# Performance work log

Measured on AMD Instinct MI355X. Metric: run time of the kernel, lower is better.

## Reference

```python
import jax, jax.numpy as jnp
import numpy as np

V, L, D, DEMO, HID, N = 20000, 128, 256, 70, 1024, 2048


def setup_inputs() -> dict:
    key = jax.random.key(0)
    ks = jax.random.split(key, 16)
    s = 1.0 / np.sqrt(D)
    inp = {
        # learned parameters
        "E": jax.random.normal(ks[0], (V, D), jnp.float32) * 0.02,
        "Wq": jax.random.normal(ks[1], (D, D), jnp.float32) * s,
        "Wk": jax.random.normal(ks[2], (D, D), jnp.float32) * s,
        "Wv": jax.random.normal(ks[3], (D, D), jnp.float32) * s,
        "c_attn": jnp.ones((1,), jnp.float32) * 0.1,   # time_weight_net coefficient (attention decay)
        "c_pool": jnp.ones((1,), jnp.float32) * 0.5,   # history_repr Q_base-style pooling decay
        "W1": jax.random.normal(ks[4], (D + DEMO, HID), jnp.float32) * (1.0 / np.sqrt(D + DEMO)),
        "b1": jnp.zeros((HID,), jnp.float32),
        "W2": jax.random.normal(ks[5], (HID, 1), jnp.float32) * (1.0 / np.sqrt(HID)),
        "b2": jnp.zeros((1,), jnp.float32),
        # batched ragged task instances
        "demo": jax.random.normal(ks[6], (N, DEMO), jnp.float32),
        "hist_times": jax.random.uniform(ks[7], (N, L), jnp.float32) * 10.0,
        "event_time": jax.random.uniform(ks[8], (N,), jnp.float32) * 10.0 + 10.0,
        "labels": jax.random.randint(ks[9], (N,), 0, 2).astype(jnp.float32),
        "codes": jax.random.randint(ks[10], (N, L), 0, V),
        "lengths": jax.random.randint(ks[11], (N,), 1, L + 1).astype(jnp.int32),
    }
    return inp


def reference(E, Wq, Wk, Wv, c_attn, c_pool, W1, b1, W2, b2,
              demo, hist_times, event_time, labels, codes, lengths):
    POS_WEIGHT = 2.0
    NEG = jnp.float32(-1e9)
    mask = jnp.arange(L)[None, :] < lengths[:, None]            # [N, L] valid history positions

    emb = E[codes]                                              # [N, L, D] gather
    q = jnp.einsum('nld,de->nle', emb, Wq)
    k = jnp.einsum('nld,de->nle', emb, Wk)
    v = jnp.einsum('nld,de->nle', emb, Wv)

    # time-aware self-attention over each ragged history (masked)
    scores = jnp.einsum('nid,njd->nij', q, k) / jnp.sqrt(jnp.float32(D))
    dt = jnp.abs(hist_times[:, :, None] - hist_times[:, None, :])  # [N, L, L]
    scores = scores - c_attn[0] * dt
    scores = jnp.where(mask[:, None, :], scores, NEG)
    attn = jax.nn.softmax(scores, axis=-1)
    events = jnp.einsum('nij,njd->nid', attn, v)                # [N, L, D]

    # history_repr: time-decayed pooling toward event_time
    w = -c_pool[0] * (event_time[:, None] - hist_times)         # [N, L]
    w = jnp.where(mask, w, NEG)
    w = jax.nn.softmax(w, axis=-1)
    repr_ = jnp.einsum('nl,nld->nd', w, events)                 # [N, D]

    # disease/death classifier: demographics + history repr -> logit
    x = jnp.concatenate([demo, repr_], axis=-1)                 # [N, DEMO+D]
    h = jax.nn.relu(x @ W1 + b1)
    logit = (h @ W2 + b2)[:, 0]                                 # [N]

    # BCEWithLogitsLoss with pos_weight, averaged over valid predictions
    loss = -(POS_WEIGHT * labels * jax.nn.log_sigmoid(logit)
             + (1.0 - labels) * jax.nn.log_sigmoid(-logit))
    avg_loss = jnp.mean(loss)

    reg_loss = jnp.sum(c_attn ** 2) + jnp.sum(c_pool ** 2)      # time_weight_net.get_reg_loss()
    return avg_loss + reg_loss
```

## Files before the change

kernel.cpp:

```cpp
#include <hip/hip_runtime.h>
#include <hip/hip_bf16.h>
#include <math.h>
#include <stdint.h>

#define VV 20000
#define LL 128
#define DD 256
#define DEMO_ 70
#define HID_ 1024
#define NN 2048

typedef __attribute__((ext_vector_type(8))) short short8;
typedef __attribute__((ext_vector_type(4))) float f32x4;

__device__ __forceinline__ float bf2f(uint32_t u) {
    union { uint32_t u; float f; } c; c.u = u << 16; return c.f;
}
__device__ __forceinline__ uint32_t f2bf(float f) {
    union { float f; uint32_t u; } c; c.f = f;
    return (c.u + 0x7fffu + ((c.u >> 16) & 1u)) >> 16;
}

__device__ __forceinline__ int sw_off(int row, int col) {
    return (row << 8) + ((((col >> 3) ^ (row & 7)) << 3) | (col & 7));
}

__global__ __launch_bounds__(256) void k_pre(
    const float* __restrict__ Wq, const float* __restrict__ Wk,
    const float* __restrict__ Wv, const float* __restrict__ W1,
    const float* __restrict__ ca, const float* __restrict__ cp,
    const int* __restrict__ lens,
    unsigned short* __restrict__ Mxf, unsigned short* __restrict__ W1f,
    int* __restrict__ order, float* __restrict__ z,
    int* __restrict__ tickets, float* __restrict__ out)
{
    __shared__ float sm[DD];
    __shared__ float wvs[8][DD];
    __shared__ int cnt[9], off[9], cur[9];
    const int b = blockIdx.x, t = threadIdx.x;

    if (b < 256) {
        int e = b;
        sm[t] = Wq[(size_t)e * DD + t];
        __syncthreads();
        const float4* wk4 = (const float4*)(Wk + (size_t)t * DD);
        const float4* wq4 = (const float4*)sm;
        float4 acc = make_float4(0.f, 0.f, 0.f, 0.f);
        #pragma unroll 8
        for (int c = 0; c < DD / 4; ++c) {
            float4 a = wq4[c]; float4 bb = wk4[c];
            acc.x += a.x * bb.x; acc.y += a.y * bb.y;
            acc.z += a.z * bb.z; acc.w += a.w * bb.w;
        }
        float val = acc.x + acc.y + acc.z + acc.w;
        int frag = (e >> 4) * 8 + (t >> 5);
        int pos  = (((t >> 3) & 3) * 16 + (e & 15)) * 8 + (t & 7);
        Mxf[(size_t)frag * 512 + pos] = (unsigned short)f2bf(val);
    } else if (b < 384) {
        int f = b - 256, kg = f >> 2, hh = f & 3;
        #pragma unroll
        for (int r = 0; r < 8; ++r)
            wvs[r][t] = Wv[(size_t)(kg * 8 + r) * DD + t];
        __syncthreads();
        int h = hh * 256 + t;
        float acc[8];
        #pragma unroll
        for (int r = 0; r < 8; ++r) acc[r] = 0.f;
        #pragma unroll 4
        for (int n = 0; n < DD; ++n) {
            float a = W1[(size_t)(DEMO_ + n) * HID_ + h];
            #pragma unroll
            for (int r = 0; r < 8; ++r) acc[r] += wvs[r][n] * a;
        }
        #pragma unroll
        for (int r = 0; r < 8; ++r) {
            int k = DEMO_ + kg * 8 + r;
            int frag = (h >> 4) * 11 + (k >> 5);
            int pos  = (((k >> 3) & 3) * 16 + (h & 15)) * 8 + (k & 7);
            W1f[(size_t)frag * 512 + pos] = (unsigned short)f2bf(acc[r]);
        }
    } else if (b < 416) {
        int g = b - 384;
        for (int idx = g * 256 + t; idx < 96 * 1024; idx += 32 * 256) {
            int kk = idx >> 10, h = idx & 1023;
            int k = kk < DEMO_ ? kk : kk + 256;
            float val = kk < DEMO_ ? W1[(size_t)kk * HID_ + h] : 0.f;
            int frag = (h >> 4) * 11 + (k >> 5);
            int pos  = (((k >> 3) & 3) * 16 + (h & 15)) * 8 + (k & 7);
            W1f[(size_t)frag * 512 + pos] = (unsigned short)f2bf(val);
        }
    } else {
        for (int i = t; i < NN; i += 256) z[i] = 0.f;
        if (t < 128) tickets[t] = 0;
        if (t < 9) cnt[t] = 0;
        __syncthreads();
        for (int i = t; i < NN; i += 256)
            atomicAdd(&cnt[(lens[i] + 15) >> 4], 1);
        __syncthreads();
        if (t == 0) {
            int acc = 0;
            for (int k = 8; k >= 1; --k) { off[k] = acc; acc += cnt[k]; cur[k] = off[k]; }
            out[0] = ca[0] * ca[0] + cp[0] * cp[0];
        }
        __syncthreads();
        for (int i = t; i < NN; i += 256) {
            int key = (lens[i] + 15) >> 4;
            int pos = atomicAdd(&cur[key], 1);
            order[pos] = i;
        }
    }
}

__global__ __launch_bounds__(512, 4) void k_main(
    const float* __restrict__ E,
    const float* __restrict__ ht,  const float* __restrict__ evt_t,
    const int* __restrict__ codes, const int* __restrict__ lens,
    const float* __restrict__ ca_p, const float* __restrict__ cp_p,
    const unsigned short* __restrict__ Mxf,
    const int* __restrict__ order,
    unsigned short* __restrict__ Rbf)
{
    __shared__ __align__(16) unsigned short emb_u[LL * DD];
    __shared__ float times_s[LL];
    __shared__ int   codes_s[LL];
    __shared__ float w_s[LL];
    __shared__ float apart[8][LL];
    __shared__ float rp_part[8][DD];
    __shared__ float asum[LL];

    const int n = order[blockIdx.x];
    const int tid = threadIdx.x, wv = tid >> 6, ln = tid & 63;
    const int q = ln >> 4, m = ln & 15;
    const int len = lens[n];
    const int it_n = (len + 15) >> 4;
    const float ca = ca_p[0], cp = cp_p[0];
    const float evt = evt_t[n];

    short8 bB[2][8];
    #pragma unroll
    for (int nt = 0; nt < 2; ++nt)
        #pragma unroll
        for (int kk = 0; kk < 8; ++kk)
            bB[nt][kk] = *(const short8*)(Mxf + (size_t)((wv * 2 + nt) * 8 + kk) * 512 + ln * 8);

    if (tid < LL) {
        bool v = tid < len;
        times_s[tid] = v ? ht[(size_t)n * LL + tid] : 0.f;
        codes_s[tid] = v ? codes[(size_t)n * LL + tid] : 0;
    }
    if (wv == 0) {
        float t0 = (ln      < len) ? ht[(size_t)n * LL + ln]      : 0.f;
        float t1 = (ln + 64 < len) ? ht[(size_t)n * LL + ln + 64] : 0.f;
        float e0 = (ln      < len) ? __expf(cp * (t0 - evt)) : 0.f;
        float e1 = (ln + 64 < len) ? __expf(cp * (t1 - evt)) : 0.f;
        float smm = e0 + e1;
        for (int o = 32; o; o >>= 1) smm += __shfl_xor(smm, o, 64);
        float inv = 1.f / smm;
        if (ln      < len) w_s[ln]      = e0 * inv;
        if (ln + 64 < len) w_s[ln + 64] = e1 * inv;
    }
    __syncthreads();

    for (int l0 = wv; l0 < len; l0 += 32) {
        float4 v[4];
        #pragma unroll
        for (int u = 0; u < 4; ++u) {
            int l = l0 + u * 8;
            if (l < len)
                v[u] = ((const float4*)(E + (size_t)codes_s[l] * DD))[ln];
        }
        #pragma unroll
        for (int u = 0; u < 4; ++u) {
            int l = l0 + u * 8;
            if (l < len)
                *(uint2*)&emb_u[sw_off(l, 4 * ln)] =
                    make_uint2(f2bf(v[u].x) | (f2bf(v[u].y) << 16),
                               f2bf(v[u].z) | (f2bf(v[u].w) << 16));
        }
    }
    __syncthreads();

    short8 aC[8];
    for (int it = 0; it < it_n; ++it) {
        f32x4 h0 = (f32x4)0.f, h1 = (f32x4)0.f;
        #pragma unroll
        for (int kk = 0; kk < 8; ++kk) {
            short8 af = *(const short8*)&emb_u[sw_off(it * 16 + m, kk * 32 + q * 8)];
            if (it == wv) aC[kk] = af;
            h0 = __builtin_amdgcn_mfma_f32_16x16x32_bf16(af, bB[0][kk], h0, 0, 0, 0);
            h1 = __builtin_amdgcn_mfma_f32_16x16x32_bf16(af, bB[1][kk], h1, 0, 0, 0);
        }
        __syncthreads();
        #pragma unroll
        for (int r = 0; r < 4; ++r) {
            int row = it * 16 + q * 4 + r;
            emb_u[sw_off(row, wv * 32 + m)]      = (unsigned short)f2bf(h0[r]);
            emb_u[sw_off(row, wv * 32 + 16 + m)] = (unsigned short)f2bf(h1[r]);
        }
    }
    __syncthreads();

    if (wv < it_n) {
        f32x4 sac[8];
        #pragma unroll
        for (int jt = 0; jt < 8; ++jt) sac[jt] = (f32x4)0.f;
        for (int jt = 0; jt < it_n; ++jt) {
            #pragma unroll
            for (int kk = 0; kk < 8; ++kk) {
                short8 bH = *(const short8*)&emb_u[sw_off(jt * 16 + m, kk * 32 + q * 8)];
                sac[jt] = __builtin_amdgcn_mfma_f32_16x16x32_bf16(aC[kk], bH, sac[jt], 0, 0, 0);
            }
        }
        int i_base = wv * 16 + q * 4;
        float ti[4]; bool vR[4]; float rowsum[4];
        #pragma unroll
        for (int r = 0; r < 4; ++r) {
            vR[r] = (i_base + r) < len;
            ti[r] = times_s[i_base + r];
            rowsum[r] = 0.f;
        }
        for (int jt = 0; jt < it_n; ++jt) {
            int jcol = jt * 16 + m;
            bool vC = jcol < len;
            float tj = times_s[jcol];
            #pragma unroll
            for (int r = 0; r < 4; ++r) {
                float arg = sac[jt][r] * 0.0625f - ca * fabsf(ti[r] - tj);
                float p = (vR[r] && vC) ? __expf(arg) : 0.f;
                sac[jt][r] = p;
                rowsum[r] += p;
            }
        }
        #pragma unroll
        for (int r = 0; r < 4; ++r) {
            float s = rowsum[r];
            s += __shfl_xor(s, 1, 64); s += __shfl_xor(s, 2, 64);
            s += __shfl_xor(s, 4, 64); s += __shfl_xor(s, 8, 64);
            rowsum[r] = s;
        }
        float sc[4];
        #pragma unroll
        for (int r = 0; r < 4; ++r)
            sc[r] = (vR[r] && rowsum[r] > 0.f) ? w_s[i_base + r] / rowsum[r] : 0.f;
        for (int jt = 0; jt < it_n; ++jt) {
            float v = sc[0] * sac[jt][0] + sc[1] * sac[jt][1]
                    + sc[2] * sac[jt][2] + sc[3] * sac[jt][3];
            v += __shfl_xor(v, 16, 64);
            v += __shfl_xor(v, 32, 64);
            if (q == 0) apart[wv][jt * 16 + m] = v;
        }
    }
    __syncthreads();

    if (tid < LL) {
        float s = 0.f;
        for (int r = 0; r < it_n; ++r) s += apart[r][tid];
        asum[tid] = s;
    }
    __syncthreads();

    if (wv < it_n) {
        float aw = asum[wv * 16 + m];
        #pragma unroll
        for (int kk = 0; kk < 8; ++kk) {
            float v[8];
            #pragma unroll
            for (int j = 0; j < 8; ++j)
                v[j] = aw * bf2f((uint32_t)(unsigned short)aC[kk][j]);
            #pragma unroll
            for (int o = 1; o <= 8; o <<= 1)
                #pragma unroll
                for (int j = 0; j < 8; ++j)
                    v[j] += __shfl_xor(v[j], o, 64);
            if (m < 8)
                rp_part[wv][kk * 32 + q * 8 + m] = v[m];
        }
    }
    __syncthreads();
    if (tid < DD) {
        float r = 0.f;
        for (int t2 = 0; t2 < it_n; ++t2) r += rp_part[t2][tid];
        Rbf[(size_t)n * DD + tid] = (unsigned short)f2bf(r);
    }
}

__global__ __launch_bounds__(256) void k_mlp(
    const float* __restrict__ demo, const float* __restrict__ labels,
    const float* __restrict__ b1,   const float* __restrict__ W2,
    const float* __restrict__ b2,
    const unsigned short* __restrict__ Rbf,
    const unsigned short* __restrict__ W1f,
    float* __restrict__ z, int* __restrict__ tickets,
    float* __restrict__ out)
{
    __shared__ __align__(16) unsigned short xs[16][360];
    __shared__ float W2s[256];
    __shared__ float b1s[256];
    __shared__ float wred[4][16];
    __shared__ int   lastflag;

    const int tid = threadIdx.x, wv = tid >> 6, ln = tid & 63;
    const int q = ln >> 4, m = ln & 15;
    const int sg = blockIdx.x;
    const int s0 = sg * 16;
    const int by = blockIdx.y;
    const int hbase = by * 256;

    W2s[tid] = W2[hbase + tid];
    b1s[tid] = b1[hbase + tid];
    {
        int sh = tid >> 6, lane = tid & 63;
        for (int s = sh; s < 16; s += 4) {
            int n_s = s0 + s;
            const uint32_t* rsrc = (const uint32_t*)(Rbf + (size_t)n_s * DD);
            ((uint32_t*)&xs[s][DEMO_])[lane]      = rsrc[lane];
            ((uint32_t*)&xs[s][DEMO_])[lane + 64] = rsrc[lane + 64];
            if (lane < 35) {
                float2 d = ((const float2*)(demo + (size_t)n_s * DEMO_))[lane];
                xs[s][2 * lane]     = (unsigned short)f2bf(d.x);
                xs[s][2 * lane + 1] = (unsigned short)f2bf(d.y);
            }
            if (lane < 17) ((uint32_t*)&xs[s][326])[lane] = 0;
        }
    }
    __syncthreads();

    f32x4 cacc[4];
    #pragma unroll
    for (int ntl = 0; ntl < 4; ++ntl) cacc[ntl] = (f32x4)0.f;

    for (int kk = 0; kk < 11; ++kk) {
        short8 af = *(const short8*)&xs[m][kk * 32 + q * 8];
        #pragma unroll
        for (int ntl = 0; ntl < 4; ++ntl) {
            int frag = (by * 16 + wv * 4 + ntl) * 11 + kk;
            short8 bfd = *(const short8*)(W1f + (size_t)frag * 512 + ln * 8);
            cacc[ntl] = __builtin_amdgcn_mfma_f32_16x16x32_bf16(af, bfd, cacc[ntl], 0, 0, 0);
        }
    }

    float ls0 = 0.f, ls1 = 0.f, ls2 = 0.f, ls3 = 0.f;
    #pragma unroll
    for (int ntl = 0; ntl < 4; ++ntl) {
        int hl = wv * 64 + ntl * 16 + m;
        float bb = b1s[hl], w2v = W2s[hl];
        ls0 += fmaxf(cacc[ntl][0] + bb, 0.f) * w2v;
        ls1 += fmaxf(cacc[ntl][1] + bb, 0.f) * w2v;
        ls2 += fmaxf(cacc[ntl][2] + bb, 0.f) * w2v;
        ls3 += fmaxf(cacc[ntl][3] + bb, 0.f) * w2v;
    }
    #pragma unroll
    for (int o = 1; o <= 8; o <<= 1) {
        ls0 += __shfl_xor(ls0, o, 64); ls1 += __shfl_xor(ls1, o, 64);
        ls2 += __shfl_xor(ls2, o, 64); ls3 += __shfl_xor(ls3, o, 64);
    }
    if (m == 0) {
        wred[wv][q * 4 + 0] = ls0; wred[wv][q * 4 + 1] = ls1;
        wred[wv][q * 4 + 2] = ls2; wred[wv][q * 4 + 3] = ls3;
    }
    __syncthreads();
    if (tid < 16)
        atomicAdd(&z[s0 + tid], wred[0][tid] + wred[1][tid] + wred[2][tid] + wred[3][tid]);
    __syncthreads();

    if (tid == 0) {
        __threadfence();
        int ticket = atomicAdd(&tickets[sg], 1);
        lastflag = (ticket == 3);
    }
    __syncthreads();
    if (lastflag && wv == 0) {
        float loss = 0.f;
        if (ln < 16) {
            float zz = atomicAdd(&z[s0 + ln], 0.f) + b2[0];
            float y = labels[s0 + ln];
            float lg = log1pf(__expf(-fabsf(zz)));
            loss = 2.f * y * (fmaxf(-zz, 0.f) + lg)
                 + (1.f - y) * (fmaxf(zz, 0.f) + lg);
        }
        #pragma unroll
        for (int o = 1; o <= 8; o <<= 1) loss += __shfl_xor(loss, o, 64);
        if (ln == 0) atomicAdd(out, loss * (1.f / (float)NN));
    }
}

extern "C" void kernel_launch(void* const* d_in, const int* in_sizes, int n_in,
                              void* d_out, int out_size, void* d_ws, size_t ws_size,
                              hipStream_t stream) {
    const float* E      = (const float*)d_in[0];
    const float* Wq     = (const float*)d_in[1];
    const float* Wk     = (const float*)d_in[2];
    const float* Wv     = (const float*)d_in[3];
    const float* ca     = (const float*)d_in[4];
    const float* cp     = (const float*)d_in[5];
    const float* W1     = (const float*)d_in[6];
    const float* b1     = (const float*)d_in[7];
    const float* W2     = (const float*)d_in[8];
    const float* b2     = (const float*)d_in[9];
    const float* demo   = (const float*)d_in[10];
    const float* ht     = (const float*)d_in[11];
    const float* evt    = (const float*)d_in[12];
    const float* labels = (const float*)d_in[13];
    const int*   codes  = (const int*)d_in[14];
    const int*   lens   = (const int*)d_in[15];
    float* out = (float*)d_out;

    unsigned short* Mxf = (unsigned short*)d_ws;
    unsigned short* W1f = (unsigned short*)((char*)d_ws + 131072);
    unsigned short* Rbf = (unsigned short*)((char*)d_ws + 851968);
    float*          zar = (float*)((char*)d_ws + 1900544);
    int*            ord = (int*)((char*)d_ws + 1908736);
    int*            tks = (int*)((char*)d_ws + 1916928);

    hipLaunchKernelGGL(k_pre,  dim3(417), dim3(256), 0, stream,
                       Wq, Wk, Wv, W1, ca, cp, lens, Mxf, W1f, ord, zar, tks, out);
    hipLaunchKernelGGL(k_main, dim3(NN), dim3(512), 0, stream,
                       E, ht, evt, codes, lens, ca, cp, Mxf, ord, Rbf);
    hipLaunchKernelGGL(k_mlp,  dim3(NN / 16, 4), dim3(256), 0, stream,
                       demo, labels, b1, W2, b2, Rbf, W1f, zar, tks, out);
}
```

Measured before the change: 226.5 us.

## Split attention column tiles across idle waves for short histories

When a history is short, fewer than eight 16-row tiles exist, so most of the eight waves used to sit idle during the score, softmax and pooling phases. Now each row tile is assigned to several waves, and each wave handles a strided subset of column tiles and of the D chunks. Row sums are combined through a new shared psum array with an extra barrier. The partial buffers are zeroed up front and summed over all eight slots, which adds a sync and some LDS traffic in exchange for better wave utilisation.

```diff
diff --git a/kernel.cpp b/kernel.cpp
--- a/kernel.cpp
+++ b/kernel.cpp
@@ -127,6 +127,7 @@
     __shared__ float apart[8][LL];
     __shared__ float rp_part[8][DD];
     __shared__ float asum[LL];
+    __shared__ float psum[8][16];
 
     const int n = order[blockIdx.x];
     const int tid = threadIdx.x, wv = tid >> 6, ln = tid & 63;
@@ -136,12 +137,24 @@
     const float ca = ca_p[0], cp = cp_p[0];
     const float evt = evt_t[n];
 
+    const int wsh = (it_n <= 1) ? 3 : (it_n == 2) ? 2 : (it_n <= 4) ? 1 : 0;
+    const int wpt = 1 << wsh;
+    const int tt = wv >> wsh, ss = wv & (wpt - 1);
+    const bool act = tt < it_n;
+
     short8 bB[2][8];
     #pragma unroll
     for (int nt = 0; nt < 2; ++nt)
         #pragma unroll
         for (int kk = 0; kk < 8; ++kk)
             bB[nt][kk] = *(const short8*)(Mxf + (size_t)((wv * 2 + nt) * 8 + kk) * 512 + ln * 8);
+
+    ((float*)apart)[tid]          = 0.f;
+    ((float*)apart)[tid + 512]    = 0.f;
+    ((float*)rp_part)[tid]        = 0.f;
+    ((float*)rp_part)[tid + 512]  = 0.f;
+    ((float*)rp_part)[tid + 1024] = 0.f;
+    ((float*)rp_part)[tid + 1536] = 0.f;
 
     if (tid < LL) {
         bool v = tid < len;
@@ -186,7 +199,7 @@
         #pragma unroll
         for (int kk = 0; kk < 8; ++kk) {
             short8 af = *(const short8*)&emb_u[sw_off(it * 16 + m, kk * 32 + q * 8)];
-            if (it == wv) aC[kk] = af;
+            if (it == tt) aC[kk] = af;
             h0 = __builtin_amdgcn_mfma_f32_16x16x32_bf16(af, bB[0][kk], h0, 0, 0, 0);
             h1 = __builtin_amdgcn_mfma_f32_16x16x32_bf16(af, bB[1][kk], h1, 0, 0, 0);
         }
@@ -200,35 +213,45 @@
     }
     __syncthreads();
 
-    if (wv < it_n) {
-        f32x4 sac[8];
-        #pragma unroll
-        for (int jt = 0; jt < 8; ++jt) sac[jt] = (f32x4)0.f;
-        for (int jt = 0; jt < it_n; ++jt) {
-            #pragma unroll
-            for (int kk = 0; kk < 8; ++kk) {
-                short8 bH = *(const short8*)&emb_u[sw_off(jt * 16 + m, kk * 32 + q * 8)];
-                sac[jt] = __builtin_amdgcn_mfma_f32_16x16x32_bf16(aC[kk], bH, sac[jt], 0, 0, 0);
+    f32x4 sac[8];
+    #pragma unroll
+    for (int j2 = 0; j2 < 8; ++j2) sac[j2] = (f32x4)0.f;
+    int i_base = tt * 16 + q * 4;
+    float ti[4]; bool vR[4]; float rowsum[4];
+    #pragma unroll
+    for (int r = 0; r < 4; ++r) rowsum[r] = 0.f;
+
+    if (act) {
+        #pragma unroll
+        for (int j2 = 0; j2 < 8; ++j2) {
+            int jt = ss + j2 * wpt;
+            if (jt < it_n) {
+                #pragma unroll
+                for (int kk = 0; kk < 8; ++kk) {
+                    short8 bH = *(const short8*)&emb_u[sw_off(jt * 16 + m, kk * 32 + q * 8)];
+                    sac[j2] = __builtin_amdgcn_mfma_f32_16x16x32_bf16(aC[kk], bH, sac[j2], 0, 0, 0);
+                }
             }
         }
-        int i_base = wv * 16 + q * 4;
-        float ti[4]; bool vR[4]; float rowsum[4];
         #pragma unroll
         for (int r = 0; r < 4; ++r) {
             vR[r] = (i_base + r) < len;
             ti[r] = times_s[i_base + r];
-            rowsum[r] = 0.f;
-        }
-        for (int jt = 0; jt < it_n; ++jt) {
-            int jcol = jt * 16 + m;
-            bool vC = jcol < len;
-            float tj = times_s[jcol];
-            #pragma unroll
-            for (int r = 0; r < 4; ++r) {
-                float arg = sac[jt][r] * 0.0625f - ca * fabsf(ti[r] - tj);
-                float p = (vR[r] && vC) ? __expf(arg) : 0.f;
-                sac[jt][r] = p;
-                rowsum[r] += p;
+        }
+        #pragma unroll
+        for (int j2 = 0; j2 < 8; ++j2) {
+            int jt = ss + j2 * wpt;
+            if (jt < it_n) {
+                int jcol = jt * 16 + m;
+                bool vC = jcol < len;
+                float tj = times_s[jcol];
+                #pragma unroll
+                for (int r = 0; r < 4; ++r) {
+                    float arg = sac[j2][r] * 0.0625f - ca * fabsf(ti[r] - tj);
+                    float p = (vR[r] && vC) ? __expf(arg) : 0.f;
+                    sac[j2][r] = p;
+                    rowsum[r] += p;
+                }
             }
         }
         #pragma unroll
@@ -238,48 +261,69 @@
             s += __shfl_xor(s, 4, 64); s += __shfl_xor(s, 8, 64);
             rowsum[r] = s;
         }
+        if (m == 0) {
+            #pragma unroll
+            for (int r = 0; r < 4; ++r) psum[wv][q * 4 + r] = rowsum[r];
+        }
+    }
+    __syncthreads();
+
+    if (act) {
         float sc[4];
         #pragma unroll
-        for (int r = 0; r < 4; ++r)
-            sc[r] = (vR[r] && rowsum[r] > 0.f) ? w_s[i_base + r] / rowsum[r] : 0.f;
-        for (int jt = 0; jt < it_n; ++jt) {
-            float v = sc[0] * sac[jt][0] + sc[1] * sac[jt][1]
-                    + sc[2] * sac[jt][2] + sc[3] * sac[jt][3];
-            v += __shfl_xor(v, 16, 64);
-            v += __shfl_xor(v, 32, 64);
-            if (q == 0) apart[wv][jt * 16 + m] = v;
+        for (int r = 0; r < 4; ++r) {
+            float tot = 0.f;
+            for (int s2 = 0; s2 < wpt; ++s2) tot += psum[tt * wpt + s2][q * 4 + r];
+            sc[r] = (vR[r] && tot > 0.f) ? w_s[i_base + r] / tot : 0.f;
+        }
+        #pragma unroll
+        for (int j2 = 0; j2 < 8; ++j2) {
+            int jt = ss + j2 * wpt;
+            if (jt < it_n) {
+                float v = sc[0] * sac[j2][0] + sc[1] * sac[j2][1]
+                        + sc[2] * sac[j2][2] + sc[3] * sac[j2][3];
+                v += __shfl_xor(v, 16, 64);
+                v += __shfl_xor(v, 32, 64);
+                if (q == 0) apart[wv][jt * 16 + m] = v;
+            }
         }
     }
     __syncthreads();
 
     if (tid < LL) {
         float s = 0.f;
-        for (int r = 0; r < it_n; ++r) s += apart[r][tid];
+        #pragma unroll
+        for (int r = 0; r < 8; ++r) s += apart[r][tid];
         asum[tid] = s;
     }
     __syncthreads();
 
-    if (wv < it_n) {
-        float aw = asum[wv * 16 + m];
+    if (act) {
+        float aw = asum[tt * 16 + m];
+        int kcnt = 8 >> wsh;
+        int kk0 = ss * kcnt, kk1 = kk0 + kcnt;
         #pragma unroll
         for (int kk = 0; kk < 8; ++kk) {
-            float v[8];
-            #pragma unroll
-            for (int j = 0; j < 8; ++j)
-                v[j] = aw * bf2f((uint32_t)(unsigned short)aC[kk][j]);
-            #pragma unroll
-            for (int o = 1; o <= 8; o <<= 1)
+            if (kk >= kk0 && kk < kk1) {
+                float v[8];
                 #pragma unroll
                 for (int j = 0; j < 8; ++j)
-                    v[j] += __shfl_xor(v[j], o, 64);
-            if (m < 8)
-                rp_part[wv][kk * 32 + q * 8 + m] = v[m];
+                    v[j] = aw * bf2f((uint32_t)(unsigned short)aC[kk][j]);
+                #pragma unroll
+                for (int o = 1; o <= 8; o <<= 1)
+                    #pragma unroll
+                    for (int j = 0; j < 8; ++j)
+                        v[j] += __shfl_xor(v[j], o, 64);
+                if (m < 8)
+                    rp_part[wv][kk * 32 + q * 8 + m] = v[m];
+            }
         }
     }
     __syncthreads();
     if (tid < DD) {
         float r = 0.f;
-        for (int t2 = 0; t2 < it_n; ++t2) r += rp_part[t2][tid];
+        #pragma unroll
+        for (int t2 = 0; t2 < 8; ++t2) r += rp_part[t2][tid];
         Rbf[(size_t)n * DD + tid] = (unsigned short)f2bf(r);
     }
 }
```

New measurement: 221.7 us (median of 2 runs). -2.1%, faster.
